# Performance work log

Hardware: AMD Instinct MI355X
Metric: run time of the kernel (lower is better)

## Reference

```python
import jax, jax.numpy as jnp
import numpy as np

EPS = 1e-5


def _bn(h, gamma, beta):
    # BatchNorm1d, training mode: biased batch statistics over nodes
    mu = jnp.mean(h, axis=0)
    var = jnp.mean(jnp.square(h - mu), axis=0)
    return (h - mu) * jax.lax.rsqrt(var + EPS) * gamma + beta


def setup_inputs() -> dict:
    key = jax.random.key(0)
    ks = jax.random.split(key, 12)
    N, E, D, H = 50000, 800000, 128, 256
    x = jax.random.normal(ks[0], (N, D), dtype=jnp.float32)
    edge_index = jax.random.randint(ks[1], (2, E), 0, N, dtype=jnp.int64)
    train_node_id = jax.random.randint(ks[2], (10000,), 0, N, dtype=jnp.int64)
    def lin(k, fan_in, fan_out):
        bound = 1.0 / np.sqrt(fan_in)
        return jax.random.uniform(k, (fan_in, fan_out), jnp.float32, -bound, bound)
    return {
        "x": x, "edge_index": edge_index, "train_node_id": train_node_id,
        "W1": lin(ks[3], D, H), "b1": jnp.zeros((H,), jnp.float32),
        "W2": lin(ks[4], H, H), "b2": jnp.zeros((H,), jnp.float32),
        "W3": lin(ks[5], H, H), "b3": jnp.zeros((H,), jnp.float32),
        "g1": jnp.ones((H,), jnp.float32), "be1": jnp.zeros((H,), jnp.float32),
        "g2": jnp.ones((H,), jnp.float32), "be2": jnp.zeros((H,), jnp.float32),
        "g3": jnp.ones((H,), jnp.float32), "be3": jnp.zeros((H,), jnp.float32),
        "Wl": lin(ks[6], H, H), "bl": jnp.zeros((H,), jnp.float32),
        "Wf": lin(ks[7], H, 1), "bf": jnp.zeros((1,), jnp.float32),
    }


def reference(x, edge_index, train_node_id, W1, b1, W2, b2, W3, b3,
              g1, be1, g2, be2, g3, be3, Wl, bl, Wf, bf):
    N = x.shape[0]
    loops = jnp.arange(N, dtype=edge_index.dtype)
    row = jnp.concatenate([edge_index[0], loops])  # destinations
    col = jnp.concatenate([edge_index[1], loops])  # sources
    deg = jax.ops.segment_sum(jnp.ones_like(row, dtype=x.dtype), row, num_segments=N)
    d_isqrt = jax.lax.rsqrt(deg)  # deg >= 1 due to self loops
    norm = (d_isqrt[row] * d_isqrt[col])[:, None]  # [E+N, 1]

    def gcn(h, W, b):
        hW = h @ W
        agg = jax.ops.segment_sum(hW[col] * norm, row, num_segments=N)
        return agg + b

    h = jax.nn.relu(_bn(gcn(x, W1, b1), g1, be1))
    h = jax.nn.relu(_bn(gcn(h, W2, b2), g2, be2))
    h = jax.nn.relu(_bn(gcn(h, W3, b3), g3, be3))
    h = jax.nn.relu(h @ Wl + bl)
    h = h[train_node_id]
    return jnp.squeeze(h @ Wf + bf, -1)
```

## Files before the change

### kernel.cpp

```cpp
#include <hip/hip_runtime.h>

typedef unsigned short u16;
typedef unsigned char u8;
typedef __attribute__((ext_vector_type(8))) short short8;
typedef __attribute__((ext_vector_type(4))) float f32x4;

#define GPB 25
#define SCAP 8

#define DEVFN static __device__ __forceinline__

DEVFN u16 f2b(float f) {
    union { float f; unsigned v; } x; x.f = f;
    unsigned r = x.v + 0x7fffu + ((x.v >> 16) & 1u);
    return (u16)(r >> 16);
}

DEVFN int detect64(const int* __restrict__ p) {
    int orv = 0;
#pragma unroll
    for (int i = 1; i < 64; i += 2) orv |= p[i];
    return (orv == 0) ? 1 : 0;
}

DEVFN unsigned get_xcc() {
    unsigned x;
    asm volatile("s_getreg_b32 %0, hwreg(HW_REG_XCC_ID)" : "=s"(x));
    return x & 7u;
}

DEVFN void accum_row8(short8 v, float* acc) {
    const unsigned* u = (const unsigned*)&v;
#pragma unroll
    for (int k = 0; k < 4; k++) {
        union { float f; unsigned w; } lo, hi;
        lo.w = u[k] << 16;
        hi.w = u[k] & 0xffff0000u;
        acc[2 * k] += lo.f;
        acc[2 * k + 1] += hi.f;
    }
}

__global__ void k_init(const float* __restrict__ W1, const float* __restrict__ W2,
                       const float* __restrict__ W3, const float* __restrict__ Wl,
                       u16* __restrict__ T1, u16* __restrict__ T2,
                       u16* __restrict__ T3, u16* __restrict__ Tl,
                       int* __restrict__ z9,
                       float* __restrict__ stat, float* __restrict__ out, int N, int M) {
    int t = blockIdx.x * 256 + threadIdx.x;
    int Z = (N * 9) / 4;
    if (t < 229376) {
        const float* W; u16* T; int K; int idx;
        if (t < 32768)        { W = W1; T = T1; K = 128; idx = t; }
        else if (t < 98304)   { W = W2; T = T2; K = 256; idx = t - 32768; }
        else if (t < 163840)  { W = W3; T = T3; K = 256; idx = t - 98304; }
        else                  { W = Wl; T = Tl; K = 256; idx = t - 163840; }
        int k = idx >> 8, n = idx & 255;
        T[(size_t)n * K + k] = f2b(W[(size_t)k * 256 + n]);
    } else if (t < 229376 + Z) {
        ((int4*)z9)[t - 229376] = (int4){0, 0, 0, 0};
    } else if (t < 229376 + Z + 384) {
        ((float4*)stat)[t - 229376 - Z] = (float4){0.f, 0.f, 0.f, 0.f};
    } else if (t < 229376 + Z + 384 + (M + 3) / 4) {
        int i = (t - 229376 - Z - 384) * 4;
        if (i + 3 < M) *(float4*)(out + i) = (float4){0.f, 0.f, 0.f, 0.f};
        else for (int k = i; k < M; k++) out[k] = 0.f;
    }
}

__global__ void k_fill(const int* __restrict__ ei, unsigned* __restrict__ cntp,
                       int* __restrict__ ovfc, u16* __restrict__ slotp,
                       u16* __restrict__ ovf, int E, int N) {
    int fl = detect64(ei);
    unsigned xcc = get_xcc();
    size_t pbase = (size_t)xcc * N;
    int t = blockIdx.x * 256 + threadIdx.x;
    int e0 = t * 2;
    if (e0 >= E) return;
    int r0, r1, c0, c1;
    bool two = (e0 + 1 < E);
    if (fl) {
        const int4* p4 = (const int4*)ei;
        int4 d = p4[t];
        int4 s = p4[(E >> 1) + t];
        r0 = d.x; r1 = d.z; c0 = s.x; c1 = s.z;
    } else {
        const int2* p2 = (const int2*)ei;
        int2 d = p2[t];
        int2 s = p2[(E >> 1) + t];
        r0 = d.x; r1 = d.y; c0 = s.x; c1 = s.y;
    }
    {
        unsigned p = __hip_atomic_fetch_add(&cntp[pbase + r0], 1u,
                                            __ATOMIC_RELAXED, __HIP_MEMORY_SCOPE_WORKGROUP);
        if (p < SCAP) slotp[(pbase + r0) * SCAP + p] = (u16)c0;
        else { int q = atomicAdd(&ovfc[r0], 1); if (q < 64) ovf[(size_t)r0 * 64 + q] = (u16)c0; }
    }
    if (two) {
        unsigned p = __hip_atomic_fetch_add(&cntp[pbase + r1], 1u,
                                            __ATOMIC_RELAXED, __HIP_MEMORY_SCOPE_WORKGROUP);
        if (p < SCAP) slotp[(pbase + r1) * SCAP + p] = (u16)c1;
        else { int q = atomicAdd(&ovfc[r1], 1); if (q < 64) ovf[(size_t)r1 * 64 + q] = (u16)c1; }
    }
}

__global__ __launch_bounds__(256) void k_prep(
        const unsigned* __restrict__ cntp, const int* __restrict__ ovfc,
        const u16* __restrict__ slotp, int* __restrict__ cnt,
        u16* __restrict__ slots, u16* __restrict__ ovf,
        const float* __restrict__ x, float* __restrict__ disq,
        u16* __restrict__ xb, int N, int CB) {
    int b = blockIdx.x;
    if (b < CB) {
        int lane = threadIdx.x & 63;
        int wv = threadIdx.x >> 6;
        int ns = lane >> 3;
        int sh = lane & 7;
        int d = b * 32 + wv * 8 + ns;
        if (d >= N) return;
        size_t po = (size_t)sh * N + d;
        int craw = (int)cntp[po];
        int cl = min(craw, SCAP);
        short8 cell = *(const short8*)(slotp + po * SCAP);
        const u16* ep = (const u16*)&cell;
        int s = cl;
#pragma unroll
        for (int i = 1; i < 8; i <<= 1) {
            int v = __shfl_up(s, i, 64);
            if (sh >= i) s += v;
        }
        int P = s - cl;
        int avail = __shfl(s, lane | 7, 64);
        int spilled = min(ovfc[d], 64);
        u16* sd = slots + (size_t)d * 32;
        u16* ovp = ovf + (size_t)d * 64;
#pragma unroll
        for (int i = 0; i < SCAP; i++) {
            if (i < cl) {
                int pos = P + i;
                u16 val = ep[i];
                if (pos < 32) sd[pos] = val;
                else { int qq = spilled + pos - 32; if (qq < 64) ovp[qq] = val; }
            }
        }
        if (sh == 7) {
            int selfpos = avail;
            if (selfpos < 32) sd[selfpos] = (u16)d;
            else { int qq = spilled + selfpos - 32; if (qq < 64) ovp[qq] = (u16)d; }
            int dc = min(avail + 1, 32);
            int tot = min(avail + 1 + spilled, dc + 64);
            cnt[d] = dc | (tot << 8);
        }
    } else {
        int tt = (b - CB) * 256 + threadIdx.x;
        if (tt >= N * 32) return;
        int row = tt >> 5;
        int l = tt & 31;
        int s = (l < 8) ? (int)cntp[(size_t)l * N + row] : 0;
        s += __shfl_xor(s, 1, 64);
        s += __shfl_xor(s, 2, 64);
        s += __shfl_xor(s, 4, 64);
        s += __shfl_xor(s, 8, 64);
        s += __shfl_xor(s, 16, 64);
        float dq = rsqrtf((float)(s + 1));
        if (l == 0) disq[row] = dq;
        int f0 = l * 4;
        float4 vx = *(const float4*)(x + (size_t)row * 128 + f0);
        ushort4 o;
        o.x = f2b(vx.x * dq); o.y = f2b(vx.y * dq); o.z = f2b(vx.z * dq); o.w = f2b(vx.w * dq);
        *(ushort4*)(xb + (size_t)(f0 >> 5) * N * 32 + (size_t)row * 32 + (f0 & 31)) = o;
    }
}

template<int PBITS>
__global__ __launch_bounds__(256) void k_gatherP(
        const u16* __restrict__ src, const int* __restrict__ cnt,
        const u16* __restrict__ slots, const u16* __restrict__ ovf,
        const float* __restrict__ disq, u16* __restrict__ dst, int N) {
    const int NP = 1 << PBITS;
    const size_t N32 = (size_t)N * 32;
    int plane = blockIdx.x & (NP - 1);
    int lane = threadIdx.x & 63;
    int wv = threadIdx.x >> 6;
    int j = lane >> 2;
    int piece = lane & 3;
    int dbase = (blockIdx.x >> PBITS) * 64 + wv * 16;
    int d = dbase + j;
    bool live = d < N;
    int packed = live ? cnt[d] : 0;
    int dc = packed & 0xff;
    int tot = packed >> 8;
    float di = live ? disq[d] : 0.f;

    short8 sb = *(const short8*)(slots + (size_t)dbase * 32 + lane * 8);
    const unsigned* sbw = (const unsigned*)&sb;

    const u16* sbase = src + (size_t)plane * N32 + piece * 8;
    const u16* ov = ovf + (size_t)d * 64;

    float acc[8] = {0.f, 0.f, 0.f, 0.f, 0.f, 0.f, 0.f, 0.f};

    int m = dc;
    m = max(m, __shfl_xor(m, 4, 64));
    m = max(m, __shfl_xor(m, 8, 64));
    m = max(m, __shfl_xor(m, 16, 64));
    m = max(m, __shfl_xor(m, 32, 64));

    for (int rb = 0; rb < 4; rb++) {
        int r0 = rb * 8;
        if (r0 >= m) break;
        int srcl = j * 4 + rb;
        int cs[8];
#pragma unroll
        for (int rw = 0; rw < 4; rw++) {
            unsigned w = (unsigned)__shfl((int)sbw[rw], srcl, 64);
#pragma unroll
            for (int hh = 0; hh < 2; hh++) {
                int r = r0 + rw * 2 + hh;
                u16 s = hh ? (u16)(w >> 16) : (u16)(w & 0xffffu);
                cs[rw * 2 + hh] = (r < dc) ? (int)s : -1;
            }
        }
        short8 vs[8];
#pragma unroll
        for (int k = 0; k < 8; k++)
            if (cs[k] >= 0) vs[k] = *(const short8*)(sbase + (size_t)cs[k] * 32);
#pragma unroll
        for (int k = 0; k < 8; k++)
            if (cs[k] >= 0) accum_row8(vs[k], acc);
    }

    int nov = tot - dc;
    int novm = nov;
    novm = max(novm, __shfl_xor(novm, 4, 64));
    novm = max(novm, __shfl_xor(novm, 8, 64));
    novm = max(novm, __shfl_xor(novm, 16, 64));
    novm = max(novm, __shfl_xor(novm, 32, 64));
    for (int r = 0; r < novm; r++) {
        if (r < nov) {
            int c = (int)ov[r];
            short8 v = *(const short8*)(sbase + (size_t)c * 32);
            accum_row8(v, acc);
        }
    }

    if (live) {
        short8 o;
        u16* op = (u16*)&o;
#pragma unroll
        for (int k = 0; k < 8; k++) op[k] = f2b(acc[k] * di);
        __builtin_nontemporal_store(o,
            (short8*)(dst + (size_t)plane * N32 + (size_t)d * 32 + piece * 8));
    }
}

template<int KS>
__global__ __launch_bounds__(256, 2) void k_gemm_rb(
        const u16* __restrict__ A, const u16* __restrict__ Wt,
        float* __restrict__ Cf, int PS, int Gtot,
        float* __restrict__ stat, const float* __restrict__ bias,
        const float* __restrict__ Wfp, const float* __restrict__ bfp,
        float* __restrict__ outp) {
    constexpr int K = KS * 32;
    __shared__ float sbuf[4][2][64];
    int wv = threadIdx.x >> 6;
    int lane = threadIdx.x & 63;
    int quad = lane >> 4;
    int mr = lane & 15;
    int colbase = blockIdx.y * 64;
    int g0 = blockIdx.x * GPB;

    short8 Bf[4][KS];
#pragma unroll
    for (int j = 0; j < 4; j++)
#pragma unroll
        for (int s = 0; s < KS; s++)
            Bf[j][s] = *(const short8*)(Wt + (size_t)(colbase + j * 16 + mr) * K + s * 32 + quad * 8);

    float4 bv4[4], wf4[4];
    if (Wfp) {
#pragma unroll
        for (int j = 0; j < 4; j++) {
            bv4[j] = *(const float4*)(bias + colbase + j * 16 + quad * 4);
            wf4[j] = *(const float4*)(Wfp + colbase + j * 16 + quad * 4);
        }
    }

    f32x4 sreg[4], s2reg[4];
#pragma unroll
    for (int j = 0; j < 4; j++) {
        sreg[j] = (f32x4){0.f, 0.f, 0.f, 0.f};
        s2reg[j] = (f32x4){0.f, 0.f, 0.f, 0.f};
    }

    for (int g = wv; g < GPB; g += 4) {
        int gg = g0 + g;
        if (gg >= Gtot) continue;
        int row = gg * 16 + mr;
        const u16* Ap = A + (size_t)row * 32 + quad * 8;

        short8 Af[KS];
#pragma unroll
        for (int s = 0; s < KS; s++) Af[s] = *(const short8*)(Ap + (size_t)s * PS);

        f32x4 acc[4];
#pragma unroll
        for (int j = 0; j < 4; j++) acc[j] = (f32x4){0.f, 0.f, 0.f, 0.f};
#pragma unroll
        for (int s = 0; s < KS; s++)
#pragma unroll
            for (int j = 0; j < 4; j++)
                acc[j] = __builtin_amdgcn_mfma_f32_16x16x32_bf16(Bf[j][s], Af[s], acc[j], 0, 0, 0);

        if (Wfp) {
            float pr = 0.f;
#pragma unroll
            for (int j = 0; j < 4; j++) {
                const float* bj = (const float*)&bv4[j];
                const float* wj = (const float*)&wf4[j];
#pragma unroll
                for (int r = 0; r < 4; r++) {
                    float v = fmaxf(acc[j][r] + bj[r], 0.f);
                    pr += v * wj[r];
                }
            }
            pr += __shfl_xor(pr, 16, 64);
            pr += __shfl_xor(pr, 32, 64);
            if (quad == 0) {
                float v = pr;
                if (blockIdx.y == 0) v += bfp[0];
                atomicAdd(&outp[row], v);
            }
            continue;
        }

        float* cp = Cf + (size_t)row * 256 + colbase + quad * 4;
#pragma unroll
        for (int j = 0; j < 4; j++) {
            *(f32x4*)(cp + j * 16) = acc[j];
            sreg[j] += acc[j];
            s2reg[j] += acc[j] * acc[j];
        }
    }

    if (stat) {
#pragma unroll
        for (int j = 0; j < 4; j++) {
#pragma unroll
            for (int r = 0; r < 4; r++) {
                float a = sreg[j][r], b = s2reg[j][r];
                a += __shfl_xor(a, 1, 64); b += __shfl_xor(b, 1, 64);
                a += __shfl_xor(a, 2, 64); b += __shfl_xor(b, 2, 64);
                a += __shfl_xor(a, 4, 64); b += __shfl_xor(b, 4, 64);
                a += __shfl_xor(a, 8, 64); b += __shfl_xor(b, 8, 64);
                if (mr == 0) {
                    sbuf[wv][0][j * 16 + quad * 4 + r] = a;
                    sbuf[wv][1][j * 16 + quad * 4 + r] = b;
                }
            }
        }
        __syncthreads();
        int t = threadIdx.x;
        if (t < 128) {
            int which = t >> 6, c = t & 63;
            float v = sbuf[0][which][c] + sbuf[1][which][c] +
                      sbuf[2][which][c] + sbuf[3][which][c];
            atomicAdd(&stat[which * 256 + colbase + c], v);
        }
    }
}


__global__ void k_bnapply(const float* __restrict__ t, const float* __restrict__ stat,
                          const float* __restrict__ gamma, const float* __restrict__ beta,
                          u16* __restrict__ h, int N, float invN,
                          const float* __restrict__ scale) {
    size_t tt = (size_t)blockIdx.x * 256 + threadIdx.x;
    size_t base = tt * 4;
    if (base >= (size_t)N * 256) return;
    int f0 = (int)(base & 255);
    int row = (int)(base >> 8);
    float sc2 = scale ? scale[row] : 1.0f;
    float4 v = *(const float4*)(t + base);
    float r[4] = {v.x, v.y, v.z, v.w};
    ushort4 o;
    u16* op = (u16*)&o;
#pragma unroll
    for (int j = 0; j < 4; j++) {
        int f = f0 + j;
        float mean = stat[f] * invN;
        float var = stat[256 + f] * invN - mean * mean;
        float rstd = rsqrtf(var + 1e-5f);
        float sc = rstd * gamma[f];
        float sh = beta[f] - mean * sc;
        op[j] = f2b(fmaxf(r[j] * sc + sh, 0.0f) * sc2);
    }
    *(ushort4*)(h + (size_t)(f0 >> 5) * N * 32 + (size_t)row * 32 + (f0 & 31)) = o;
}

__global__ void k_bnapply_idx(const float* __restrict__ t, const float* __restrict__ stat,
                              const float* __restrict__ gamma, const float* __restrict__ beta,
                              const int* __restrict__ idx, u16* __restrict__ zin,
                              int M, float invN) {
    int fl = detect64(idx);
    size_t tt = (size_t)blockIdx.x * 256 + threadIdx.x;
    size_t base = tt * 4;
    if (base >= (size_t)M * 256) return;
    int f0 = (int)(base & 255);
    int row = (int)(base >> 8);
    int node = idx[(size_t)row << fl];
    float4 v = *(const float4*)(t + (size_t)node * 256 + f0);
    float r[4] = {v.x, v.y, v.z, v.w};
    ushort4 o;
    u16* op = (u16*)&o;
#pragma unroll
    for (int j = 0; j < 4; j++) {
        int f = f0 + j;
        float mean = stat[f] * invN;
        float var = stat[256 + f] * invN - mean * mean;
        float rstd = rsqrtf(var + 1e-5f);
        float sc = rstd * gamma[f];
        float sh = beta[f] - mean * sc;
        op[j] = f2b(fmaxf(r[j] * sc + sh, 0.0f));
    }
    *(ushort4*)(zin + (size_t)(f0 >> 5) * M * 32 + (size_t)row * 32 + (f0 & 31)) = o;
}


extern "C" void kernel_launch(void* const* d_in, const int* in_sizes, int n_in,
                              void* d_out, int out_size, void* d_ws, size_t ws_size,
                              hipStream_t stream) {
    const int D = 128, H = 256;
    const int N = in_sizes[0] / D;
    const int E = in_sizes[1] / 2;
    const int M = in_sizes[2];

    const float* x = (const float*)d_in[0];
    const int* ei = (const int*)d_in[1];
    const int* tnid = (const int*)d_in[2];
    const float* W1 = (const float*)d_in[3];
    const float* W2 = (const float*)d_in[5];
    const float* W3 = (const float*)d_in[7];
    const float* g1 = (const float*)d_in[9];
    const float* be1 = (const float*)d_in[10];
    const float* g2 = (const float*)d_in[11];
    const float* be2 = (const float*)d_in[12];
    const float* g3 = (const float*)d_in[13];
    const float* be3 = (const float*)d_in[14];
    const float* Wl = (const float*)d_in[15];
    const float* bl = (const float*)d_in[16];
    const float* Wf = (const float*)d_in[17];
    const float* bfp = (const float*)d_in[18];
    float* out = (float*)d_out;

    char* w = (char*)d_ws;
    size_t off = 0;
    auto carve = [&](size_t bytes) -> void* {
        void* p = w + off;
        off = (off + bytes + 255) & ~(size_t)255;
        return p;
    };

    float* stat = (float*)carve(3 * 512 * 4);
    float* disq = (float*)carve((size_t)N * 4);
    int* cnt = (int*)carve((size_t)N * 4);
    u16* slots = (u16*)carve((size_t)N * 32 * 2);
    u16* ovf = (u16*)carve((size_t)N * 64 * 2);
    u16* Wt1 = (u16*)carve((size_t)H * D * 2);
    u16* Wt2 = (u16*)carve((size_t)H * H * 2);
    u16* Wt3 = (u16*)carve((size_t)H * H * 2);
    u16* Wtl = (u16*)carve((size_t)H * H * 2);
    u16* xb = (u16*)carve((size_t)N * D * 2);
    u16* aggx = (u16*)carve((size_t)N * D * 2);
    u16* aggh = (u16*)carve((size_t)N * H * 2);
    float* tb = (float*)carve((size_t)N * H * 4);
    u16* hb = (u16*)carve((size_t)N * H * 2);
    u16* zin = (u16*)carve((size_t)M * H * 2);

    unsigned* cntp = (unsigned*)tb;
    int* ovfc = (int*)(cntp + (size_t)8 * N);
    u16* slotp = (u16*)(ovfc + N);

    const float invN = 1.0f / (float)N;

    const int Gn = N / 16;
    const int Gm = M / 16;
    dim3 gemm_grid((Gn + GPB - 1) / GPB, 4);
    dim3 gemm_grid_m((Gm + GPB - 1) / GPB, 4);
    const int PSn = N * 32;
    const int PSm = M * 32;
    const int chunks = (N + 63) / 64;
    const int PB = (int)(((size_t)N * H / 4 + 255) / 256);
    const int PBm = (int)(((size_t)M * H / 4 + 255) / 256);
    const int CB = (N + 31) / 32;
    const int XB = (N * 32 + 255) / 256;
    const int initT = 229376 + (N * 9) / 4 + 384 + (M + 3) / 4;

    k_init<<<(initT + 255) / 256, 256, 0, stream>>>(
        W1, W2, W3, Wl, Wt1, Wt2, Wt3, Wtl, (int*)cntp, stat, out, N, M);
    k_fill<<<(E / 2 + 255) / 256, 256, 0, stream>>>(ei, cntp, ovfc, slotp, ovf, E, N);
    k_prep<<<CB + XB, 256, 0, stream>>>(cntp, ovfc, slotp, cnt, slots, ovf, x, disq, xb, N, CB);

    k_gatherP<2><<<4 * chunks, 256, 0, stream>>>(xb, cnt, slots, ovf, disq, aggx, N);
    k_gemm_rb<4><<<gemm_grid, 256, 0, stream>>>(aggx, Wt1, tb, PSn, Gn, stat, nullptr, nullptr, nullptr, nullptr);
    k_bnapply<<<PB, 256, 0, stream>>>(tb, stat, g1, be1, hb, N, invN, disq);
    k_gatherP<3><<<8 * chunks, 256, 0, stream>>>(hb, cnt, slots, ovf, disq, aggh, N);
    k_gemm_rb<8><<<gemm_grid, 256, 0, stream>>>(aggh, Wt2, tb, PSn, Gn, stat + 512, nullptr, nullptr, nullptr, nullptr);
    k_bnapply<<<PB, 256, 0, stream>>>(tb, stat + 512, g2, be2, hb, N, invN, disq);
    k_gatherP<3><<<8 * chunks, 256, 0, stream>>>(hb, cnt, slots, ovf, disq, aggh, N);
    k_gemm_rb<8><<<gemm_grid, 256, 0, stream>>>(aggh, Wt3, tb, PSn, Gn, stat + 1024, nullptr, nullptr, nullptr, nullptr);
    k_bnapply_idx<<<PBm, 256, 0, stream>>>(tb, stat + 1024, g3, be3, tnid, zin, M, invN);

    k_gemm_rb<8><<<gemm_grid_m, 256, 0, stream>>>(zin, Wtl, nullptr, PSm, Gm, nullptr, bl, Wf, bfp, out);
}
```

Baseline: 401.4 us.

## Mask layer-3 GEMM stores to train nodes, prefetch A fragments, shrink gather batches

Builds a byte mask of train node ids in k_fill. The layer-3 GEMM then writes its fp32 output only for rows that the final indexed BN reads, while still accumulating BN statistics over every row. This removes most of the N x 256 fp32 store traffic. The GEMM loop also software-prefetches the next group's A fragments into registers, and the gather loop now issues batches of 4 neighbour rows instead of 8. These changes add register pressure in the GEMM and make the gather issue less memory-level parallelism per iteration.

```diff
diff --git a/kernel.cpp b/kernel.cpp
--- a/kernel.cpp
+++ b/kernel.cpp
@@ -46,9 +46,11 @@
                        u16* __restrict__ T1, u16* __restrict__ T2,
                        u16* __restrict__ T3, u16* __restrict__ Tl,
                        int* __restrict__ z9,
+                       u8* __restrict__ bm,
                        float* __restrict__ stat, float* __restrict__ out, int N, int M) {
     int t = blockIdx.x * 256 + threadIdx.x;
     int Z = (N * 9) / 4;
+    int BMC = N / 16;
     if (t < 229376) {
         const float* W; u16* T; int K; int idx;
         if (t < 32768)        { W = W1; T = T1; K = 128; idx = t; }
@@ -59,10 +61,12 @@
         T[(size_t)n * K + k] = f2b(W[(size_t)k * 256 + n]);
     } else if (t < 229376 + Z) {
         ((int4*)z9)[t - 229376] = (int4){0, 0, 0, 0};
-    } else if (t < 229376 + Z + 384) {
-        ((float4*)stat)[t - 229376 - Z] = (float4){0.f, 0.f, 0.f, 0.f};
-    } else if (t < 229376 + Z + 384 + (M + 3) / 4) {
-        int i = (t - 229376 - Z - 384) * 4;
+    } else if (t < 229376 + Z + BMC) {
+        ((int4*)bm)[t - 229376 - Z] = (int4){0, 0, 0, 0};
+    } else if (t < 229376 + Z + BMC + 384) {
+        ((float4*)stat)[t - 229376 - Z - BMC] = (float4){0.f, 0.f, 0.f, 0.f};
+    } else if (t < 229376 + Z + BMC + 384 + (M + 3) / 4) {
+        int i = (t - 229376 - Z - BMC - 384) * 4;
         if (i + 3 < M) *(float4*)(out + i) = (float4){0.f, 0.f, 0.f, 0.f};
         else for (int k = i; k < M; k++) out[k] = 0.f;
     }
@@ -70,11 +74,17 @@
 
 __global__ void k_fill(const int* __restrict__ ei, unsigned* __restrict__ cntp,
                        int* __restrict__ ovfc, u16* __restrict__ slotp,
-                       u16* __restrict__ ovf, int E, int N) {
+                       u16* __restrict__ ovf, const int* __restrict__ tnid,
+                       u8* __restrict__ bm, int E, int N, int M) {
     int fl = detect64(ei);
     unsigned xcc = get_xcc();
     size_t pbase = (size_t)xcc * N;
     int t = blockIdx.x * 256 + threadIdx.x;
+    if (t < M) {
+        int fl2 = detect64(tnid);
+        int node = tnid[(size_t)t << fl2];
+        bm[node] = 1;
+    }
     int e0 = t * 2;
     if (e0 >= E) return;
     int r0, r1, c0, c1;
@@ -206,14 +216,15 @@
     m = max(m, __shfl_xor(m, 16, 64));
     m = max(m, __shfl_xor(m, 32, 64));
 
-    for (int rb = 0; rb < 4; rb++) {
-        int r0 = rb * 8;
+    for (int rb = 0; rb < 8; rb++) {
+        int r0 = rb * 4;
         if (r0 >= m) break;
-        int srcl = j * 4 + rb;
-        int cs[8];
-#pragma unroll
-        for (int rw = 0; rw < 4; rw++) {
-            unsigned w = (unsigned)__shfl((int)sbw[rw], srcl, 64);
+        int srcl = j * 4 + (rb >> 1);
+        int w0 = (rb & 1) * 2;
+        int cs[4];
+#pragma unroll
+        for (int rw = 0; rw < 2; rw++) {
+            unsigned w = (unsigned)__shfl((int)sbw[w0 + rw], srcl, 64);
 #pragma unroll
             for (int hh = 0; hh < 2; hh++) {
                 int r = r0 + rw * 2 + hh;
@@ -221,12 +232,12 @@
                 cs[rw * 2 + hh] = (r < dc) ? (int)s : -1;
             }
         }
-        short8 vs[8];
-#pragma unroll
-        for (int k = 0; k < 8; k++)
+        short8 vs[4];
+#pragma unroll
+        for (int k = 0; k < 4; k++)
             if (cs[k] >= 0) vs[k] = *(const short8*)(sbase + (size_t)cs[k] * 32);
 #pragma unroll
-        for (int k = 0; k < 8; k++)
+        for (int k = 0; k < 4; k++)
             if (cs[k] >= 0) accum_row8(vs[k], acc);
     }
 
@@ -258,7 +269,8 @@
 __global__ __launch_bounds__(256, 2) void k_gemm_rb(
         const u16* __restrict__ A, const u16* __restrict__ Wt,
         float* __restrict__ Cf, int PS, int Gtot,
-        float* __restrict__ stat, const float* __restrict__ bias,
+        float* __restrict__ stat, const u8* __restrict__ wmask,
+        const float* __restrict__ bias,
         const float* __restrict__ Wfp, const float* __restrict__ bfp,
         float* __restrict__ outp) {
     constexpr int K = KS * 32;
@@ -293,15 +305,28 @@
         s2reg[j] = (f32x4){0.f, 0.f, 0.f, 0.f};
     }
 
+    short8 Afc[KS];
+    {
+        const u16* Ap = A + (size_t)((g0 + wv) * 16 + mr) * 32 + quad * 8;
+#pragma unroll
+        for (int s = 0; s < KS; s++) Afc[s] = *(const short8*)(Ap + (size_t)s * PS);
+    }
+
     for (int g = wv; g < GPB; g += 4) {
         int gg = g0 + g;
-        if (gg >= Gtot) continue;
+        if (gg >= Gtot) break;
         int row = gg * 16 + mr;
-        const u16* Ap = A + (size_t)row * 32 + quad * 8;
-
-        short8 Af[KS];
-#pragma unroll
-        for (int s = 0; s < KS; s++) Af[s] = *(const short8*)(Ap + (size_t)s * PS);
+
+        short8 Afn[KS];
+        int gn = g + 4;
+        if (gn < GPB) {
+            const u16* Ap = A + (size_t)((g0 + gn) * 16 + mr) * 32 + quad * 8;
+#pragma unroll
+            for (int s = 0; s < KS; s++) Afn[s] = *(const short8*)(Ap + (size_t)s * PS);
+        } else {
+#pragma unroll
+            for (int s = 0; s < KS; s++) Afn[s] = Afc[s];
+        }
 
         f32x4 acc[4];
 #pragma unroll
@@ -310,7 +335,7 @@
         for (int s = 0; s < KS; s++)
 #pragma unroll
             for (int j = 0; j < 4; j++)
-                acc[j] = __builtin_amdgcn_mfma_f32_16x16x32_bf16(Bf[j][s], Af[s], acc[j], 0, 0, 0);
+                acc[j] = __builtin_amdgcn_mfma_f32_16x16x32_bf16(Bf[j][s], Afc[s], acc[j], 0, 0, 0);
 
         if (Wfp) {
             float pr = 0.f;
@@ -331,16 +356,19 @@
                 if (blockIdx.y == 0) v += bfp[0];
                 atomicAdd(&outp[row], v);
             }
-            continue;
-        }
-
-        float* cp = Cf + (size_t)row * 256 + colbase + quad * 4;
-#pragma unroll
-        for (int j = 0; j < 4; j++) {
-            *(f32x4*)(cp + j * 16) = acc[j];
-            sreg[j] += acc[j];
-            s2reg[j] += acc[j] * acc[j];
-        }
+        } else {
+            bool wr = !wmask || wmask[row];
+            float* cp = Cf + (size_t)row * 256 + colbase + quad * 4;
+#pragma unroll
+            for (int j = 0; j < 4; j++) {
+                if (wr) *(f32x4*)(cp + j * 16) = acc[j];
+                sreg[j] += acc[j];
+                s2reg[j] += acc[j] * acc[j];
+            }
+        }
+
+#pragma unroll
+        for (int s = 0; s < KS; s++) Afc[s] = Afn[s];
     }
 
     if (stat) {
@@ -476,6 +504,7 @@
     float* tb = (float*)carve((size_t)N * H * 4);
     u16* hb = (u16*)carve((size_t)N * H * 2);
     u16* zin = (u16*)carve((size_t)M * H * 2);
+    u8* bm = (u8*)carve((size_t)N);
 
     unsigned* cntp = (unsigned*)tb;
     int* ovfc = (int*)(cntp + (size_t)8 * N);
@@ -494,22 +523,22 @@
     const int PBm = (int)(((size_t)M * H / 4 + 255) / 256);
     const int CB = (N + 31) / 32;
     const int XB = (N * 32 + 255) / 256;
-    const int initT = 229376 + (N * 9) / 4 + 384 + (M + 3) / 4;
+    const int initT = 229376 + (N * 9) / 4 + N / 16 + 384 + (M + 3) / 4;
 
     k_init<<<(initT + 255) / 256, 256, 0, stream>>>(
-        W1, W2, W3, Wl, Wt1, Wt2, Wt3, Wtl, (int*)cntp, stat, out, N, M);
-    k_fill<<<(E / 2 + 255) / 256, 256, 0, stream>>>(ei, cntp, ovfc, slotp, ovf, E, N);
+        W1, W2, W3, Wl, Wt1, Wt2, Wt3, Wtl, (int*)cntp, bm, stat, out, N, M);
+    k_fill<<<(E / 2 + 255) / 256, 256, 0, stream>>>(ei, cntp, ovfc, slotp, ovf, tnid, bm, E, N, M);
     k_prep<<<CB + XB, 256, 0, stream>>>(cntp, ovfc, slotp, cnt, slots, ovf, x, disq, xb, N, CB);
 
     k_gatherP<2><<<4 * chunks, 256, 0, stream>>>(xb, cnt, slots, ovf, disq, aggx, N);
-    k_gemm_rb<4><<<gemm_grid, 256, 0, stream>>>(aggx, Wt1, tb, PSn, Gn, stat, nullptr, nullptr, nullptr, nullptr);
+    k_gemm_rb<4><<<gemm_grid, 256, 0, stream>>>(aggx, Wt1, tb, PSn, Gn, stat, nullptr, nullptr, nullptr, nullptr, nullptr);
     k_bnapply<<<PB, 256, 0, stream>>>(tb, stat, g1, be1, hb, N, invN, disq);
     k_gatherP<3><<<8 * chunks, 256, 0, stream>>>(hb, cnt, slots, ovf, disq, aggh, N);
-    k_gemm_rb<8><<<gemm_grid, 256, 0, stream>>>(aggh, Wt2, tb, PSn, Gn, stat + 512, nullptr, nullptr, nullptr, nullptr);
+    k_gemm_rb<8><<<gemm_grid, 256, 0, stream>>>(aggh, Wt2, tb, PSn, Gn, stat + 512, nullptr, nullptr, nullptr, nullptr, nullptr);
     k_bnapply<<<PB, 256, 0, stream>>>(tb, stat + 512, g2, be2, hb, N, invN, disq);
     k_gatherP<3><<<8 * chunks, 256, 0, stream>>>(hb, cnt, slots, ovf, disq, aggh, N);
-    k_gemm_rb<8><<<gemm_grid, 256, 0, stream>>>(aggh, Wt3, tb, PSn, Gn, stat + 1024, nullptr, nullptr, nullptr, nullptr);
+    k_gemm_rb<8><<<gemm_grid, 256, 0, stream>>>(aggh, Wt3, tb, PSn, Gn, stat + 1024, bm, nullptr, nullptr, nullptr, nullptr);
     k_bnapply_idx<<<PBm, 256, 0, stream>>>(tb, stat + 1024, g3, be3, tnid, zin, M, invN);
 
-    k_gemm_rb<8><<<gemm_grid_m, 256, 0, stream>>>(zin, Wtl, nullptr, PSm, Gm, nullptr, bl, Wf, bfp, out);
-}
+    k_gemm_rb<8><<<gemm_grid_m, 256, 0, stream>>>(zin, Wtl, nullptr, PSm, Gm, nullptr, nullptr, bl, Wf, bfp, out);
+}
```

Result: slower. 425.1 us (+5.9%).
